# Performance work log

Hardware: AMD Instinct MI355X
Metric: run time of the kernel (lower is better)

Reference implementation:

```python
import jax, jax.numpy as jnp
from jax import lax
import numpy as np

K = 9  # nsamples = 3*3 ball-query neighbors
LAYERS = [
    dict(cin=0,    mid=45,   cout=64,   r=1.5, ss=2, tk=1, ts=1, pad=(0, 0)),
    dict(cin=64,   mid=96,   cout=128,  r=3.0, ss=2, tk=3, ts=2, pad=(1, 0)),
    dict(cin=128,  mid=192,  cout=256,  r=3.0, ss=1, tk=3, ts=1, pad=(1, 1)),
    dict(cin=256,  mid=384,  cout=512,  r=6.0, ss=2, tk=3, ts=2, pad=(1, 0)),
    dict(cin=512,  mid=768,  cout=1024, r=6.0, ss=1, tk=3, ts=1, pad=(1, 1)),
    dict(cin=1024, mid=1536, cout=2048, r=6.0, ss=2, tk=1, ts=1, pad=(0, 0)),
]

def furthest_point_sample(xyz, m):
    B, N, _ = xyz.shape
    def step(carry, _):
        mind, last = carry
        lastp = jnp.take_along_axis(xyz, last[:, None, None], axis=1)  # (B,1,3)
        mind = jnp.minimum(mind, jnp.sum((xyz - lastp) ** 2, axis=-1))
        nxt = jnp.argmax(mind, axis=-1).astype(jnp.int32)
        return (mind, nxt), last
    init = (jnp.full((B, N), 1e10, xyz.dtype), jnp.zeros((B,), jnp.int32))
    _, idxs = lax.scan(step, init, None, length=m)
    return jnp.swapaxes(idxs, 0, 1)

def ball_query(radius, k, points, anchors):
    # first-k-within-radius semantics of the pointnet2 CUDA ball_query kernel
    d2 = jnp.sum((anchors[:, :, None, :] - points[:, None, :, :]) ** 2, axis=-1)  # (B,M,N)
    N = points.shape[1]
    mask = d2 < radius * radius
    key = jnp.where(mask, jnp.arange(N, dtype=jnp.int32), N)
    idx = -lax.top_k(-key, k)[0]  # k smallest keys = first k in-radius indices
    first = jnp.argmax(mask, axis=-1).astype(jnp.int32)  # 0 if none in radius (CUDA init)
    return jnp.where(idx < N, idx, first[:, :, None]).astype(jnp.int32)

def pst_conv(xyzs, feats, Wd, Wf, Wt, cfg):
    # xyzs: (B,L,N,3); feats: (B,L,N,Cin) or None (channel-last layout, same math as torch (B,L,C,N))
    B, L, N, _ = xyzs.shape
    p0, p1 = cfg['pad']
    if p0 + p1:
        zx = jnp.zeros((B, 1, N, 3), xyzs.dtype)
        xyzs = jnp.concatenate([zx] * p0 + [xyzs] + [zx] * p1, axis=1)
        if feats is not None:
            zf = jnp.zeros((B, 1, N, feats.shape[-1]), feats.dtype)
            feats = jnp.concatenate([zf] * p0 + [feats] + [zf] * p1, axis=1)
    tr = cfg['tk'] // 2
    m = N // cfg['ss']
    bi = jnp.arange(B)[:, None, None]
    out_x, out_f = [], []
    for t in range(tr, xyzs.shape[1] - tr, cfg['ts']):
        aidx = furthest_point_sample(xyzs[:, t], m)
        anchor = jnp.take_along_axis(xyzs[:, t], aidx[:, :, None], axis=1)  # (B,m,3)
        parts = []
        for i in range(t - tr, t + tr + 1):
            idx = ball_query(cfg['r'], K, xyzs[:, i], anchor)   # (B,m,K)
            nb = xyzs[:, i][bi, idx]                            # (B,m,K,3) gather
            disp = nb - anchor[:, :, None, :]
            d = jnp.einsum('bmkc,oc->bmko', disp, Wd)           # 1x1 conv on displacement
            if feats is not None:
                fg = feats[:, i][bi, idx]                       # (B,m,K,Cin) gather
                sf = jnp.einsum('bmkc,oc->bmko', fg, Wf) * d    # 'multiplication' aggregation
            else:
                sf = d
            parts.append(jnp.sum(sf, axis=2))                   # 'sum' spatial pooling
        nf = jnp.concatenate(parts, axis=-1)                    # (B,m,tk*mid)
        mu = jnp.mean(nf, axis=(0, 1))
        var = jnp.var(nf, axis=(0, 1))
        nf = jax.nn.relu((nf - mu) * lax.rsqrt(var + 1e-5))     # BatchNorm1d (batch stats, affine=identity-init) + ReLU
        nf = jnp.einsum('bmc,oc->bmo', nf, Wt)                  # temporal 1x1 conv
        out_x.append(anchor)
        out_f.append(nf)
    return jnp.stack(out_x, axis=1), jnp.stack(out_f, axis=1)

def _forward(xyzs, Wds, Wfs, Wts, fc_w, fc_b):
    B, S, L, N, C = xyzs.shape
    x = xyzs.reshape(B * S, L, N, C)  # mirrors xyzs.reshape((-1, L_sub_clip, N_point, C_xyz))
    feats = None
    for li, cfg in enumerate(LAYERS):
        x, feats = pst_conv(x, feats, Wds[li], Wfs[li], Wts[li], cfg)
        if li < len(LAYERS) - 1:
            feats = jax.nn.relu(feats)  # F.relu between PSTConv blocks (not after conv4)
    tokens = jnp.einsum('blnc,oc->blno', feats, fc_w) + fc_b  # conv_fc on permuted features
    BT, Lout, M, Cout = tokens.shape  # Lout == 1 per the model's assert
    return tokens.reshape(B, S, M, Cout)

def setup_inputs() -> dict:
    key = jax.random.key(0)
    ks = iter(jax.random.split(key, 40))
    B, S, L, N = 8, 4, 4, 2048
    inp = {'xyzs': jax.random.normal(next(ks), (B, S, L, N, 3), jnp.float32), 'epoch': 1}
    def xav(k, o, i):
        gain = np.sqrt(2.0)  # relu gain, matching get_and_init_FC_layer style init
        bound = gain * np.sqrt(6.0 / (o + i))
        return jax.random.uniform(k, (o, i), jnp.float32, -bound, bound)
    for li, cfg in enumerate(LAYERS):
        inp['d%d' % li] = xav(next(ks), cfg['mid'], 3)
        if cfg['cin']:
            inp['f%d' % li] = xav(next(ks), cfg['mid'], cfg['cin'])
        inp['t%d' % li] = xav(next(ks), cfg['cout'], cfg['tk'] * cfg['mid'])
    inp['fc_w'] = xav(next(ks), 1024, 2048)
    inp['fc_b'] = jnp.zeros((1024,), jnp.float32)
    return inp

def reference(xyzs, d0, d1, d2, d3, d4, d5, f1, f2, f3, f4, f5, t0, t1, t2, t3, t4, t5, fc_w, fc_b, epoch):
    Wds = [d0, d1, d2, d3, d4, d5]
    Wfs = [None, f1, f2, f3, f4, f5]
    Wts = [t0, t1, t2, t3, t4, t5]
    return _forward(xyzs, Wds, Wfs, Wts, fc_w, fc_b)
```

## Files before the change

### kernel.cpp

```cpp
#include <hip/hip_runtime.h>
#include <hip/hip_bf16.h>
#include <math.h>

typedef __hip_bfloat16 bf16;
typedef _Float16 f16;
typedef _Float16 f16x2 __attribute__((ext_vector_type(2)));
typedef _Float16 f16x8 __attribute__((ext_vector_type(8)));
typedef float f32x4 __attribute__((ext_vector_type(4)));

struct Sched { int tt[5]; int fi[5]; int jj[5]; };
struct CvtF32 { const void* src[4]; float* dst[4]; int n[4]; int blk0[5]; };
struct CvtF16 { const void* src[6]; f16* dst[6]; int n[6]; int blk0[7]; };
struct W2J { const void* wd[5]; const void* wf[5]; f16* dst[5]; int mid[5]; int cin[5]; int n[5]; int blk0[6]; };

__global__ void k_detect(const unsigned int* __restrict__ w, int nwords, int* __restrict__ flag,
                         float* __restrict__ zp, int zn){
  if(blockIdx.x==0){
    __shared__ int cnt;
    if(threadIdx.x==0) cnt=0;
    __syncthreads();
    int local=0;
    for(int i=threadIdx.x;i<nwords;i+=256){
      unsigned int v=w[i];
      int e=(v>>7)&0xFF;
      if(e>=0xC0) local++;
    }
    atomicAdd(&cnt, local);
    __syncthreads();
    if(threadIdx.x==0) flag[0] = (cnt > (nwords>>3)) ? 1 : 0;
  } else {
    int i=(blockIdx.x-1)*256+threadIdx.x;
    if(i<zn) zp[i]=0.f;
  }
}

__device__ inline float ldmix(const void* p, size_t i, bool f32m){
  return f32m ? ((const float*)p)[i] : __bfloat162float(((const bf16*)p)[i]);
}

__global__ void k_cvt_all(CvtF32 J, const int* __restrict__ flag){
  int b=blockIdx.x;
  int j=0;
  while(j<3 && J.blk0[j+1]<=b) j++;
  int i=(b-J.blk0[j])*256+threadIdx.x;
  if(i>=J.n[j]) return;
  bool f32m=*flag!=0;
  J.dst[j][i]=ldmix(J.src[j],i,f32m);
}

__global__ __launch_bounds__(256) void k_fps0m(
    const float* __restrict__ xyz, float* __restrict__ anchors,
    CvtF16 J16, W2J JW, const int* __restrict__ flag, int cvtB)
{
  __shared__ float4 ptsS[8*256];
  __shared__ unsigned long long keyS[2][4];
  __shared__ float ancS[3*1024];
  int bid=(int)blockIdx.x;
  if(bid<128){
    const int L=4, N=2048, m=1024, T=4;
    int prob=bid;
    int b=prob/T, tt=prob%T;
    int f=tt;
    const float* src = xyz + ((size_t)(b*L+f))*N*3;
    float* anc = anchors + ((size_t)(b*T+tt))*m*3;
    int tid=threadIdx.x;
    for(int t=tid;t<N;t+=256)
      ptsS[t]=make_float4(src[3*t],src[3*t+1],src[3*t+2],0.f);
    __syncthreads();
    float px[8],py[8],pz[8],mind[8];
#pragma unroll
    for(int j=0;j<8;j++){
      float4 v=ptsS[tid+j*256];
      px[j]=v.x; py[j]=v.y; pz[j]=v.z; mind[j]=1e10f;
    }
    float4 p0=ptsS[0];
    float lx=p0.x, ly=p0.y, lz=p0.z;
    if(tid==0){ ancS[0]=lx; ancS[1]=ly; ancS[2]=lz; }
    int w=tid>>6;
    for(int it=1; it<m; ++it){
      float bv=-1.f; int bi=0;
#pragma unroll
      for(int j=0;j<8;j++){
#pragma clang fp contract(off)
        float dx=px[j]-lx, dy=py[j]-ly, dz=pz[j]-lz;
        float d2=dx*dx+dy*dy+dz*dz;
        float mv=mind[j]; if(d2<mv) mv=d2; mind[j]=mv;
        if(mv>bv){ bv=mv; bi=tid+j*256; }
      }
      unsigned int hi=__float_as_uint(bv);
      unsigned int lo=0xFFFFFFFFu-(unsigned)bi;
#define DPPSTEP(CTRL) { \
      unsigned int shi=(unsigned)__builtin_amdgcn_update_dpp(0,(int)hi,CTRL,0xF,0xF,true); \
      unsigned int slo=(unsigned)__builtin_amdgcn_update_dpp(0,(int)lo,CTRL,0xF,0xF,true); \
      bool g=(shi>hi)||(shi==hi&&slo>lo); \
      hi=g?shi:hi; lo=g?slo:lo; }
      DPPSTEP(0x111) DPPSTEP(0x112) DPPSTEP(0x114) DPPSTEP(0x118) DPPSTEP(0x142) DPPSTEP(0x143)
#undef DPPSTEP
      if((tid&63)==63)
        keyS[it&1][w]=((unsigned long long)hi<<32)|lo;
      __syncthreads();
      unsigned long long k0=keyS[it&1][0], k1=keyS[it&1][1];
      unsigned long long k2=keyS[it&1][2], k3=keyS[it&1][3];
      unsigned long long ka = k0>k1?k0:k1;
      unsigned long long kb = k2>k3?k2:k3;
      unsigned long long kk = ka>kb?ka:kb;
      int wi = (int)(0xFFFFFFFFu - (unsigned)(kk & 0xFFFFFFFFull));
      float4 wc = ptsS[wi];
      lx=wc.x; ly=wc.y; lz=wc.z;
      if(tid==0){ ancS[3*it]=lx; ancS[3*it+1]=ly; ancS[3*it+2]=lz; }
    }
    __syncthreads();
    for(int t=tid;t<3*m;t+=256) anc[t]=ancS[t];
  } else if(bid < 128+cvtB){
    int b=bid-128;
    int j=0;
    while(j<5 && J16.blk0[j+1]<=b) j++;
    int i=(b-J16.blk0[j])*256+threadIdx.x;
    if(i>=J16.n[j]) return;
    bool f32m=*flag!=0;
    J16.dst[j][i]=(f16)ldmix(J16.src[j],i,f32m);
  } else {
    int b=bid-128-cvtB;
    int j=0;
    while(j<4 && JW.blk0[j+1]<=b) j++;
    int i=(b-JW.blk0[j])*256+threadIdx.x;
    if(i>=JW.n[j]) return;
    int cin=JW.cin[j]; int K3=3*cin;
    int o=i/K3; int rem=i-o*K3; int a=rem/cin; int c=rem-a*cin;
    float v=0.f;
    if(o<JW.mid[j]){
      bool f32m=*flag!=0;
      v=ldmix(JW.wd[j],(size_t)3*o+a,f32m)*ldmix(JW.wf[j],(size_t)o*cin+c,f32m);
    }
    JW.dst[j][i]=(f16)v;
  }
}

template<int P>
__global__ __launch_bounds__(256) void k_mega(
    const float* __restrict__ xyzF, int Lf, int Nf, int mf,
    int c0,int c1,int c2,int c3, int Tf, float* __restrict__ ancOut, int fpsN,
    int oN, int isP0,
    const f16* __restrict__ featsO, const float* __restrict__ XinO, const float* __restrict__ XoutO,
    const int* __restrict__ bqO, f16* __restrict__ GoN, int mO, int cinO, int NO, int LinO,
    size_t aBSO, int MO, Sched SO, const float* __restrict__ WdO, int midO, int ldO,
    const float* __restrict__ XinB, const float* __restrict__ XoutB, int* __restrict__ bqOut,
    int NB, int mB, float r2B, int LinB, size_t aBSB, int MB, Sched SB, int chunksB)
{
  __shared__ float4 ptsS[P*256];
  __shared__ unsigned long long keyS[2][4];
  __shared__ float sp[768];
  int bid=(int)blockIdx.x;
  if(bid < fpsN){
    int prob=bid;
    int b=prob/Tf, tt=prob%Tf;
    int f=(tt==0)?c0:(tt==1)?c1:(tt==2)?c2:c3;
    const float* src = xyzF + ((size_t)(b*Lf+f))*Nf*3;
    float* anc = ancOut + ((size_t)(b*Tf+tt))*mf*3;
    int tid=threadIdx.x;
    for(int t=tid;t<Nf;t+=256)
      ptsS[t]=make_float4(src[3*t],src[3*t+1],src[3*t+2],0.f);
    __syncthreads();
    float px[P],py[P],pz[P],mind[P];
#pragma unroll
    for(int j=0;j<P;j++){
      float4 v=ptsS[tid+j*256];
      px[j]=v.x; py[j]=v.y; pz[j]=v.z; mind[j]=1e10f;
    }
    float4 p0=ptsS[0];
    float lx=p0.x, ly=p0.y, lz=p0.z;
    if(tid==0){ anc[0]=lx; anc[1]=ly; anc[2]=lz; }
    int w=tid>>6;
    for(int it=1; it<mf; ++it){
      float bv=-1.f; int bi=0;
#pragma unroll
      for(int j=0;j<P;j++){
#pragma clang fp contract(off)
        float dx=px[j]-lx, dy=py[j]-ly, dz=pz[j]-lz;
        float d2=dx*dx+dy*dy+dz*dz;
        float mv=mind[j]; if(d2<mv) mv=d2; mind[j]=mv;
        if(mv>bv){ bv=mv; bi=tid+j*256; }
      }
      unsigned int hi=__float_as_uint(bv);
      unsigned int lo=0xFFFFFFFFu-(unsigned)bi;
#define DPPSTEP(CTRL) { \
      unsigned int shi=(unsigned)__builtin_amdgcn_update_dpp(0,(int)hi,CTRL,0xF,0xF,true); \
      unsigned int slo=(unsigned)__builtin_amdgcn_update_dpp(0,(int)lo,CTRL,0xF,0xF,true); \
      bool g=(shi>hi)||(shi==hi&&slo>lo); \
      hi=g?shi:hi; lo=g?slo:lo; }
      DPPSTEP(0x111) DPPSTEP(0x112) DPPSTEP(0x114) DPPSTEP(0x118) DPPSTEP(0x142) DPPSTEP(0x143)
#undef DPPSTEP
      if((tid&63)==63)
        keyS[it&1][w]=((unsigned long long)hi<<32)|lo;
      __syncthreads();
      unsigned long long k0=keyS[it&1][0], k1=keyS[it&1][1];
      unsigned long long k2=keyS[it&1][2], k3=keyS[it&1][3];
      unsigned long long ka = k0>k1?k0:k1;
      unsigned long long kb = k2>k3?k2:k3;
      unsigned long long kk = ka>kb?ka:kb;
      int wi = (int)(0xFFFFFFFFu - (unsigned)(kk & 0xFFFFFFFFull));
      float4 wc = ptsS[wi];
      lx=wc.x; ly=wc.y; lz=wc.z;
      if(tid==0){ anc[3*it]=lx; anc[3*it+1]=ly; anc[3*it+2]=lz; }
    }
  } else if(bid < fpsN + oN){
    int ob = bid - fpsN;
    if(isP0){
      int quarter = MO>>2;
      int tt = ob / quarter, rb = ob - tt*quarter;
      int sub = threadIdx.x>>6;
      int o = threadIdx.x&63;
      int row = rb*4 + sub;
      int b = row/mO, mm = row - b*mO;
      const float* A = XoutO + (size_t)b*aBSO + (size_t)tt*mO*3 + (size_t)mm*3;
      float ax=A[0], ay=A[1], az=A[2];
      float w0=0,w1=0,w2=0;
      if(o<midO){ w0=WdO[3*o]; w1=WdO[3*o+1]; w2=WdO[3*o+2]; }
      int fr=SO.fi[tt];
      int nmask=NO-1;
      const int* id = bqO + ((size_t)tt*MO + row)*9;
      const float* Pb = XinO + ((size_t)b*LinO+fr)*(size_t)NO*3;
      float acc=0.f;
      for(int k=0;k<9;k++){
        int p=id[k] & nmask;
        const float* q = Pb + (size_t)p*3;
        float dx=q[0]-ax, dy=q[1]-ay, dz=q[2]-az;
        acc += dx*w0+dy*w1+dz*w2;
      }
      if(o<midO) GoN[(size_t)tt*MO*ldO + (size_t)row*ldO + o] = (f16)acc;
    } else {
      int cw2 = cinO>>1; if(cw2>256) cw2=256;
      int rpb = 256/cw2;
      int tid=threadIdx.x;
      int sub=tid/cw2, lc=tid-sub*cw2;
      int r=ob*rpb+sub;
      int Kp=3*cinO;
      int nmask=NO-1;
      int s=r/MO, mrow=r-s*MO;
      int b=mrow/mO, mm=mrow-b*mO;
      int tt=SO.tt[s], fr=SO.fi[s];
      const float* A0=XoutO+(size_t)b*aBSO+(size_t)tt*mO*3+(size_t)mm*3;
      float ax=A0[0],ay=A0[1],az=A0[2];
      const float* Pb=XinO+((size_t)b*LinO+fr)*(size_t)NO*3;
      const f16* Fb=featsO+(((size_t)b*LinO+fr)*(size_t)NO)*(size_t)cinO;
      const int* id=bqO+(size_t)r*9;
      int idx[9]; float d0[9],d1[9],d2a[9];
#pragma unroll
      for(int k=0;k<9;k++){
        int p=id[k]&nmask; idx[k]=p;
        const float* q=Pb+(size_t)p*3;
        d0[k]=q[0]-ax; d1[k]=q[1]-ay; d2a[k]=q[2]-az;
      }
      f16* Gr=GoN+(size_t)r*Kp;
      for(int cc=2*lc; cc<cinO; cc+=2*cw2){
        float a0=0,a1=0,a2=0,b0=0,b1=0,b2=0;
#pragma unroll
        for(int k=0;k<9;k++){
          f16x2 fv=*(const f16x2*)(Fb+(size_t)idx[k]*cinO+cc);
          float f0=(float)fv[0], f1=(float)fv[1];
          a0=fmaf(d0[k],f0,a0); b0=fmaf(d0[k],f1,b0);
          a1=fmaf(d1[k],f0,a1); b1=fmaf(d1[k],f1,b1);
          a2=fmaf(d2a[k],f0,a2); b2=fmaf(d2a[k],f1,b2);
        }
        f16x2 o0={(f16)a0,(f16)b0}, o1={(f16)a1,(f16)b1}, o2={(f16)a2,(f16)b2};
        *(f16x2*)(Gr+cc)=o0; *(f16x2*)(Gr+cinO+cc)=o1; *(f16x2*)(Gr+2*cinO+cc)=o2;
      }
    }
  } else {
    int fb=bid-fpsN-oN;
    int s=fb/(32*chunksB);
    int rem=fb-s*(32*chunksB);
    int b=rem/chunksB;
    int a=(rem-b*chunksB)*256+threadIdx.x;
    int tt=SB.tt[s], fr=SB.fi[s];
    const float* Pb = XinB + ((size_t)b*LinB + fr)*(size_t)NB*3;
    bool act = a<mB;
    float ax=0,ay=0,az=0;
    int* o = bqOut + ((size_t)s*MB + (size_t)b*mB + (size_t)(act?a:0))*9;
    if(act){
      const float* A=XoutB+(size_t)b*aBSB+(size_t)tt*mB*3+(size_t)a*3;
      ax=A[0]; ay=A[1]; az=A[2];
    }
    int cnt = act?0:9, first=0;
    for(int base=0; base<NB; base+=256){
      for(int t=threadIdx.x; t<768; t+=256) sp[t]=Pb[(size_t)base*3+t];
      __syncthreads();
      for(int q=0;q<256;q++){
#pragma clang fp contract(off)
        float dx=sp[3*q]-ax, dy=sp[3*q+1]-ay, dz=sp[3*q+2]-az;
        float d2=dx*dx+dy*dy+dz*dz;
        if(d2<r2B && cnt<9){
          int p=base+q;
          if(cnt==0) first=p;
          o[cnt]=p; cnt++;
        }
      }
      if(__syncthreads_and(cnt>=9)) break;
    }
    if(act){ for(int k=cnt;k<9;k++) o[k]=first; }
  }
}

__global__ __launch_bounds__(256) void k_outer(
    const f16* __restrict__ feats, const float* __restrict__ Xin,
    const float* __restrict__ Xout, const int* __restrict__ bqAll,
    f16* __restrict__ Gh, int m, int cin, int N, int Lin,
    size_t aBS, int nmask, int M, Sched S)
{
  int cw2 = cin>>1; if(cw2>256) cw2=256;
  int rpb = 256/cw2;
  int tid=threadIdx.x;
  int sub=tid/cw2, lc=tid-sub*cw2;
  int r=blockIdx.x*rpb+sub;
  int Kp=3*cin;
  int s=r/M, mrow=r-s*M;
  int b=mrow/m, mm=mrow-b*m;
  int tt=S.tt[s], fr=S.fi[s];
  const float* A0=Xout+(size_t)b*aBS+(size_t)tt*m*3+(size_t)mm*3;
  float ax=A0[0],ay=A0[1],az=A0[2];
  const float* Pb=Xin+((size_t)b*Lin+fr)*(size_t)N*3;
  const f16* Fb=feats+(((size_t)b*Lin+fr)*(size_t)N)*(size_t)cin;
  const int* id=bqAll+(size_t)r*9;
  int idx[9]; float d0[9],d1[9],d2a[9];
#pragma unroll
  for(int k=0;k<9;k++){
    int p=id[k]&nmask; idx[k]=p;
    const float* q=Pb+(size_t)p*3;
    d0[k]=q[0]-ax; d1[k]=q[1]-ay; d2a[k]=q[2]-az;
  }
  f16* Gr=Gh+(size_t)r*Kp;
  for(int cc=2*lc; cc<cin; cc+=2*cw2){
    float a0=0,a1=0,a2=0,b0=0,b1=0,b2=0;
#pragma unroll
    for(int k=0;k<9;k++){
      f16x2 fv=*(const f16x2*)(Fb+(size_t)idx[k]*cin+cc);
      float f0=(float)fv[0], f1=(float)fv[1];
      a0=fmaf(d0[k],f0,a0); b0=fmaf(d0[k],f1,b0);
      a1=fmaf(d1[k],f0,a1); b1=fmaf(d1[k],f1,b1);
      a2=fmaf(d2a[k],f0,a2); b2=fmaf(d2a[k],f1,b2);
    }
    f16x2 o0={(f16)a0,(f16)b0}, o1={(f16)a1,(f16)b1}, o2={(f16)a2,(f16)b2};
    *(f16x2*)(Gr+cc)=o0; *(f16x2*)(Gr+cin+cc)=o1; *(f16x2*)(Gr+2*cin+cc)=o2;
  }
}

__global__ __launch_bounds__(256) void k_pg(
    const f16* __restrict__ Gh, const f16* __restrict__ W2,
    f16* __restrict__ nfh, int Kp, int mid, int C, int M, Sched S,
    float* __restrict__ sumsL, int sumStride)
{
  __shared__ f16 As[128*40];
  __shared__ f16 Bs[128*40];
  int tid=threadIdx.x;
  int lane=tid&63, w=tid>>6;
  int quad=lane>>4, l15=lane&15;
  int rowOff=(w>>1)*64, colOff=(w&1)*64;
  int rowBase=blockIdx.x*128, colBase=blockIdx.y*128;
  f32x4 acc[4][4];
#pragma unroll
  for(int i=0;i<4;i++)
#pragma unroll
    for(int j=0;j<4;j++) acc[i][j]=(f32x4){0.f,0.f,0.f,0.f};
  int nct=Kp>>5;
  int srow=tid>>1, shalf=tid&1;
  for(int ct=0;ct<nct;ct++){
    __syncthreads();
    {
      const uint4* s=(const uint4*)(Gh+(size_t)(rowBase+srow)*Kp+(ct<<5)+(shalf<<4));
      uint4 u0=s[0], u1=s[1];
      *(uint4*)(As + srow*40 + (shalf<<4))     = u0;
      *(uint4*)(As + srow*40 + (shalf<<4) + 8) = u1;
    }
    {
      const uint4* s=(const uint4*)(W2+(size_t)(colBase+srow)*Kp+(ct<<5)+(shalf<<4));
      uint4 u0=s[0], u1=s[1];
      *(uint4*)(Bs + srow*40 + (shalf<<4))     = u0;
      *(uint4*)(Bs + srow*40 + (shalf<<4) + 8) = u1;
    }
    __syncthreads();
    f16x8 af[4], bf4[4];
#pragma unroll
    for(int rt=0;rt<4;rt++) af[rt]=*(const f16x8*)(As + (rowOff+rt*16+l15)*40 + quad*8);
#pragma unroll
    for(int ctl=0;ctl<4;ctl++) bf4[ctl]=*(const f16x8*)(Bs + (colOff+ctl*16+l15)*40 + quad*8);
#pragma unroll
    for(int rt=0;rt<4;rt++)
#pragma unroll
      for(int ctl=0;ctl<4;ctl++)
        acc[rt][ctl]=__builtin_amdgcn_mfma_f32_16x16x32_f16(af[rt],bf4[ctl],acc[rt][ctl],0,0,0);
  }
  int s0=rowBase/M;
  int tt0=S.tt[s0], j0=S.jj[s0];
#pragma unroll
  for(int ctl=0;ctl<4;ctl++){
    int gcol=colBase+colOff+ctl*16+l15;
    float cs=0.f, cq=0.f;
#pragma unroll
    for(int rt=0;rt<4;rt++)
#pragma unroll
      for(int r=0;r<4;r++){
        float v=(float)(f16)acc[rt][ctl][r];
        cs+=v; cq+=v*v;
      }
    cs+=__shfl_xor(cs,16); cq+=__shfl_xor(cq,16);
    cs+=__shfl_xor(cs,32); cq+=__shfl_xor(cq,32);
    if(quad==0 && gcol<mid){
      atomicAdd(&sumsL[tt0*sumStride + j0*mid + gcol], cs);
      atomicAdd(&sumsL[tt0*sumStride + C + j0*mid + gcol], cq);
    }
  }
#pragma unroll
  for(int rt=0;rt<4;rt++){
#pragma unroll
    for(int r=0;r<4;r++){
      int row=rowBase+rowOff+rt*16+quad*4+r;
      int s=row/M, mrow=row-s*M;
      int tt=S.tt[s], j=S.jj[s];
      f16* base = nfh + (size_t)tt*M*C + (size_t)mrow*C + j*mid;
#pragma unroll
      for(int ctl=0;ctl<4;ctl++){
        int col=colBase+colOff+ctl*16+l15;
        if(col<mid) base[col]=(f16)acc[rt][ctl][r];
      }
    }
  }
}

__global__ void k_bnstat(const f16* __restrict__ nfh, int M, int C, float* __restrict__ sumsL,
                         int mid, int4 jm, int sumStride){
  int c = blockIdx.x*256 + threadIdx.x;
  if(c>=C) return;
  int tt=blockIdx.z;
  int jmask = (tt==0)?jm.x:(tt==1)?jm.y:(tt==2)?jm.z:jm.w;
  int j=c/mid;
  if(!((jmask>>j)&1)) return;
  const f16* base=nfh+(size_t)tt*M*C;
  int rows = M>>5;
  int r0 = blockIdx.y*rows, r1 = r0+rows;
  float s=0.f, s2=0.f;
  for(int r=r0;r<r1;r++){
    float v=(float)base[(size_t)r*C+c];
    s+=v; s2+=v*v;
  }
  atomicAdd(&sumsL[tt*sumStride+c], s);
  atomicAdd(&sumsL[tt*sumStride+C+c], s2);
}

template<bool RELU, bool DYN, bool BNA>
__global__ __launch_bounds__(256) void k_gemm_mfma(
    const f16* __restrict__ Ag, const f16* __restrict__ Bh,
    const float* __restrict__ bias, void* __restrict__ out,
    int K, int N, int mloc, size_t oBS, size_t ttA, size_t ttO,
    const int* __restrict__ oflag, const float* __restrict__ sumsAll, int sumStride, float invM)
{
  __shared__ f16 As[128*40];
  __shared__ f16 Bs[128*40];
  __shared__ float scbL[BNA?2*2304:2];
  int tid=threadIdx.x;
  int lane=tid&63, w=tid>>6;
  int quad=lane>>4, l15=lane&15;
  int rowOff=(w>>1)*64, colOff=(w&1)*64;
  int rowBase=blockIdx.x*128, colBase=blockIdx.y*128;
  int tt=blockIdx.z;
  const f16* A0=Ag+(size_t)tt*ttA;
  if(BNA){
    const float* sm=sumsAll+(size_t)tt*sumStride;
    for(int c=tid;c<K;c+=256){
      float s1=sm[c], s2=sm[K+c];
      float mean=s1*invM;
      float var=s2*invM-mean*mean; if(var<0.f) var=0.f;
      float rs=(s2==0.f)?0.f:(1.0f/sqrtf(var+1e-5f));
      scbL[c]=rs; scbL[K+c]=-mean*rs;
    }
  }
  f32x4 acc[4][4];
#pragma unroll
  for(int i=0;i<4;i++)
#pragma unroll
    for(int j=0;j<4;j++) acc[i][j]=(f32x4){0.f,0.f,0.f,0.f};
  int nct=K>>5;
  int srow=tid>>1, shalf=tid&1;
  for(int ct=0;ct<nct;ct++){
    __syncthreads();
    {
      int c0g=(ct<<5)+(shalf<<4);
      const f16* src=A0+(size_t)(rowBase+srow)*K+c0g;
      if(BNA){
        f16x8 x0=((const f16x8*)src)[0], x1=((const f16x8*)src)[1];
        f16x8 h0,h1;
#pragma unroll
        for(int q=0;q<8;q++){
          h0[q]=(f16)fmaxf(fmaf((float)x0[q],scbL[c0g+q],scbL[K+c0g+q]),0.f);
          h1[q]=(f16)fmaxf(fmaf((float)x1[q],scbL[c0g+8+q],scbL[K+c0g+8+q]),0.f);
        }
        *(f16x8*)(As+srow*40+(shalf<<4))=h0;
        *(f16x8*)(As+srow*40+(shalf<<4)+8)=h1;
      } else {
        const uint4* s=(const uint4*)src;
        uint4 u0=s[0],u1=s[1];
        *(uint4*)(As+srow*40+(shalf<<4))=u0;
        *(uint4*)(As+srow*40+(shalf<<4)+8)=u1;
      }
    }
    {
      const uint4* s=(const uint4*)(Bh+(size_t)(colBase+srow)*K+(ct<<5)+(shalf<<4));
      uint4 u0=s[0], u1=s[1];
      *(uint4*)(Bs + srow*40 + (shalf<<4))     = u0;
      *(uint4*)(Bs + srow*40 + (shalf<<4) + 8) = u1;
    }
    __syncthreads();
    f16x8 af[4], bf4[4];
#pragma unroll
    for(int rt=0;rt<4;rt++) af[rt]=*(const f16x8*)(As + (rowOff+rt*16+l15)*40 + quad*8);
#pragma unroll
    for(int ctl=0;ctl<4;ctl++) bf4[ctl]=*(const f16x8*)(Bs + (colOff+ctl*16+l15)*40 + quad*8);
#pragma unroll
    for(int rt=0;rt<4;rt++)
#pragma unroll
      for(int ctl=0;ctl<4;ctl++)
        acc[rt][ctl]=__builtin_amdgcn_mfma_f32_16x16x32_f16(af[rt],bf4[ctl],acc[rt][ctl],0,0,0);
  }
  bool f32m = DYN ? (*oflag!=0) : true;
#pragma unroll
  for(int rt=0;rt<4;rt++){
#pragma unroll
    for(int r=0;r<4;r++){
      int row=rowBase+rowOff+rt*16+quad*4+r;
      int rb=row/mloc, rm=row-rb*mloc;
      size_t obase=(size_t)rb*oBS + (size_t)tt*ttO + (size_t)rm*N;
#pragma unroll
      for(int ctl=0;ctl<4;ctl++){
        int col=colBase+colOff+ctl*16+l15;
        float v=acc[rt][ctl][r];
        if(bias) v+=bias[col];
        if(RELU) v=fmaxf(v,0.f);
        if(DYN){
          if(!f32m) ((bf16*)out)[obase+col]=__float2bfloat16(v);
          else      ((float*)out)[obase+col]=v;
        } else {
          ((f16*)out)[obase+col]=(f16)v;
        }
      }
    }
  }
}

__global__ __launch_bounds__(256) void k_gemm0(
    const f16* __restrict__ nfh, const float* __restrict__ Wg,
    f16* __restrict__ out, int M, int K, int N, int mloc, size_t oBS, size_t ttO,
    const float* __restrict__ sumsAll, int sumStride, float invM)
{
  __shared__ alignas(16) float As[16][64];
  __shared__ alignas(16) float Bs[16][64];
  __shared__ float scbL[128];
  int tid=threadIdx.x, tx=tid&15, ty=tid>>4;
  int rowBase=blockIdx.x*64, colBase=blockIdx.y*64;
  int tt=blockIdx.z;
  const f16* A0=nfh+(size_t)tt*M*K;
  {
    const float* sm=sumsAll+(size_t)tt*sumStride;
    for(int c=tid;c<K;c+=256){
      float s1=sm[c], s2=sm[K+c];
      float mean=s1*invM;
      float var=s2*invM-mean*mean; if(var<0.f) var=0.f;
      float rs=(s2==0.f)?0.f:(1.0f/sqrtf(var+1e-5f));
      scbL[c]=rs; scbL[K+c]=-mean*rs;
    }
  }
  float acc[4][4];
#pragma unroll
  for(int i=0;i<4;i++)
#pragma unroll
    for(int j=0;j<4;j++) acc[i][j]=0.f;
  int lrow=tid&63, lcq=tid>>6;
  int nct=(K+15)>>4;
  for(int ct=0;ct<nct;ct++){
    __syncthreads();
    {
      int r=rowBase+lrow, c0=(ct<<4)+(lcq<<2);
#pragma unroll
      for(int q=0;q<4;q++){
        int c=c0+q;
        As[(lcq<<2)+q][lrow] = (c<K)? fmaxf(fmaf((float)A0[(size_t)r*K+c],scbL[c],scbL[K+c]),0.f) : 0.f;
      }
    }
    {
      int og=colBase+lrow, c0=(ct<<4)+(lcq<<2);
#pragma unroll
      for(int q=0;q<4;q++){
        int c=c0+q;
        Bs[(lcq<<2)+q][lrow] = (c<K)? Wg[(size_t)og*K+c] : 0.f;
      }
    }
    __syncthreads();
#pragma unroll
    for(int c=0;c<16;c++){
      float4 a4=*(const float4*)&As[c][ty<<2];
      float av[4]={a4.x,a4.y,a4.z,a4.w};
      float4 b4=*(const float4*)&Bs[c][tx<<2];
      float bw[4]={b4.x,b4.y,b4.z,b4.w};
#pragma unroll
      for(int i=0;i<4;i++)
#pragma unroll
        for(int j=0;j<4;j++) acc[i][j]+=av[i]*bw[j];
    }
  }
#pragma unroll
  for(int i=0;i<4;i++){
    int r=rowBase+(ty<<2)+i;
    int rb=r/mloc, rm=r-rb*mloc;
    size_t obase=(size_t)rb*oBS + (size_t)blockIdx.z*ttO + (size_t)rm*N;
#pragma unroll
    for(int j=0;j<4;j++){
      int o=colBase+(tx<<2)+j;
      out[obase+o]=(f16)fmaxf(acc[i][j],0.f);
    }
  }
}

extern "C" void kernel_launch(void* const* d_in, const int* in_sizes, int n_in,
                              void* d_out, int out_size, void* d_ws, size_t ws_size,
                              hipStream_t stream) {
  (void)in_sizes; (void)n_in; (void)out_size; (void)ws_size;

  const int di[6] = {2,4,7,10,13,16};
  const int fi6[6] = {-1,5,8,11,14,17};
  const int ti[6] = {3,6,9,12,15,18};

  const int midv[6]={45,96,192,384,768,1536};
  const int midp[6]={0,128,256,384,768,1536};
  const int cinv[6]={0,64,128,256,512,1024};
  const int coutv[6]={64,128,256,512,1024,2048};
  const int tkv[6]={1,3,3,3,3,1};
  const int Nv[6]={2048,1024,512,512,256,256};
  const int mv[6]={1024,512,512,256,256,128};
  const int Lv[6]={4,4,2,2,1,1};
  const int Tv[6]={4,2,2,1,1,1};
  const float rrv[6]={1.5f,3.f,3.f,6.f,6.f,6.f};

  float* ws=(float*)d_ws;
  size_t off=0;
  auto A=[&](size_t n)->float*{ float* p=ws+off; off+=(n+63)&~(size_t)63; return p; };
  auto Ah=[&](size_t n)->f16*{ return (f16*)A((n+1)/2); };

  int* flag=(int*)A(64);

  f16* W2h[6]; W2h[0]=nullptr;
  for(int l=1;l<6;l++) W2h[l]=Ah((size_t)midp[l]*3*cinv[l]);
  f16* Wth[6]; Wth[0]=nullptr;
  for(int l=1;l<6;l++) Wth[l]=Ah((size_t)coutv[l]*tkv[l]*midv[l]);
  float* Wd0=A(135);
  float* Wt0=A(2880);
  f16* fcwh=Ah(2097152);
  float* fcb=A(1024);

  float* X[7];
  X[0]=A(786432);
  for(int l=0;l<6;l++) X[l+1]=A((size_t)32*Tv[l]*mv[l]*3);

  f16* FA=Ah(8388608);
  f16* FB=Ah(8388608);
  f16* F[7]; F[0]=nullptr;
  for(int l=0;l<6;l++) F[l+1]=(l%2==0)?FA:FB;

  f16* nfh=Ah(18874368);
  float* sumsAll=A(11*4608);
  f16* Gh=Ah(25165824);
  int* bqA=(int*)A(1179648);
  int* bqB=(int*)A(1179648);
  int* bqBuf[2]={bqA,bqB};

  {
    int zn=11*4608;
    int zb=(zn+255)/256;
    k_detect<<<dim3(1+zb),dim3(256),0,stream>>>((const unsigned int*)d_in[0], 4096, flag, sumsAll, zn);
  }
  {
    CvtF32 J;
    J.src[0]=d_in[0];  J.dst[0]=X[0];  J.n[0]=786432;
    J.src[1]=d_in[3];  J.dst[1]=Wt0;   J.n[1]=2880;
    J.src[2]=d_in[20]; J.dst[2]=fcb;   J.n[2]=1024;
    J.src[3]=d_in[2];  J.dst[3]=Wd0;   J.n[3]=135;
    J.blk0[0]=0; J.blk0[1]=3072; J.blk0[2]=3084; J.blk0[3]=3088; J.blk0[4]=3089;
    k_cvt_all<<<dim3(3089),dim3(256),0,stream>>>(J,flag);
  }

  CvtF16 J16; int bp16=0;
  {
    int ns[6]={36864,147456,589824,2359296,3145728,2097152};
    const void* ss[6]={d_in[ti[1]],d_in[ti[2]],d_in[ti[3]],d_in[ti[4]],d_in[ti[5]],d_in[19]};
    f16* ds[6]={Wth[1],Wth[2],Wth[3],Wth[4],Wth[5],fcwh};
    for(int j2=0;j2<6;j2++){ J16.src[j2]=ss[j2]; J16.dst[j2]=ds[j2]; J16.n[j2]=ns[j2]; J16.blk0[j2]=bp16; bp16+=(ns[j2]+255)/256; }
    J16.blk0[6]=bp16;
  }
  W2J JW; int bpw2=0;
  {
    for(int l=1;l<6;l++){
      int j2=l-1;
      JW.wd[j2]=d_in[di[l]]; JW.wf[j2]=d_in[fi6[l]]; JW.dst[j2]=W2h[l];
      JW.mid[j2]=midv[l]; JW.cin[j2]=cinv[l]; JW.n[j2]=midp[l]*3*cinv[l];
      JW.blk0[j2]=bpw2; bpw2+=(JW.n[j2]+255)/256;
    }
    JW.blk0[5]=bpw2;
  }

  const int SLOTS[6]={4,5,4,2,1,1};
  const int sTT[6][5]={{0,1,2,3,0},{0,0,1,1,1},{0,0,1,1,0},{0,0,0,0,0},{0,0,0,0,0},{0,0,0,0,0}};
  const int sFI[6][5]={{0,1,2,3,0},{0,1,1,2,3},{0,1,0,1,0},{0,1,0,0,0},{0,0,0,0,0},{0,0,0,0,0}};
  const int sJJ[6][5]={{0,0,0,0,0},{1,2,0,1,2},{1,2,0,1,0},{1,2,0,0,0},{1,0,0,0,0},{0,0,0,0,0}};
  const int4 jm4l0={1,1,1,1};
  const int Tcenters[6][4]={{0,1,2,3},{0,2,0,0},{0,1,0,0},{0,0,0,0},{0,0,0,0},{0,0,0,0}};
  const int slotBase[6]={0,4,6,8,9,10};

  Sched Sl[6];
  for(int l=0;l<6;l++)
    for(int s=0;s<5;s++){ Sl[l].tt[s]=sTT[l][s]; Sl[l].fi[s]=sFI[l][s]; Sl[l].jj[s]=sJJ[l][s]; }

  auto bqGeo=[&](int lb, int& bqN, int& chunks){
    chunks=(mv[lb]+255)>>8;
    bqN=SLOTS[lb]*32*chunks;
  };

  k_fps0m<<<dim3((unsigned)(128+bp16+bpw2)),dim3(256),0,stream>>>(X[0],X[1],J16,JW,flag,bp16);

  {
    int bqN,chunks; bqGeo(0,bqN,chunks);
    int fpsN=32*Tv[1];
    k_mega<4><<<dim3((unsigned)(fpsN+bqN)),dim3(256),0,stream>>>(
        X[1],Lv[1],Nv[1],mv[1],Tcenters[1][0],Tcenters[1][1],Tcenters[1][2],Tcenters[1][3],Tv[1],X[2],fpsN,
        0,0, FA,X[0],X[1],bqA,nfh,mv[0],1,Nv[0],Lv[0],(size_t)Tv[0]*mv[0]*3,32*mv[0],Sl[0],Wd0,1,1,
        X[0],X[1],bqBuf[0],Nv[0],mv[0],rrv[0]*rrv[0],Lv[0],(size_t)Tv[0]*mv[0]*3,32*mv[0],Sl[0],chunks);
  }

  for(int l=0;l<6;l++){
    int N=Nv[l], m=mv[l], Lin=Lv[l], T=Tv[l], cin=cinv[l], mid=midv[l];
    int C=tkv[l]*midv[l], M=32*m, cout=coutv[l];
    size_t aBS=(size_t)T*m*3;
    float* sumsL=sumsAll+(size_t)slotBase[l]*4608;

    if(l<5){
      int lb=l+1;
      int bqN,chunksB; bqGeo(lb,bqN,chunksB);
      size_t aBSB=(size_t)Tv[lb]*mv[lb]*3;
      int MB=32*mv[lb];
      int oN, isP0;
      if(l==0){ isP0=1; oN=M; }
      else{
        isP0=0;
        int cw2=cin>>1; if(cw2>256) cw2=256;
        int rpb=256/cw2;
        oN=SLOTS[l]*M/rpb;
      }
      const f16* featsO=(l==0)?FA:F[l];
      f16* GoN=(l==0)?nfh:Gh;
      int fpsN=0, lf=l+2;
      if(lf<=5) fpsN=32*Tv[lf];
      int a0=0,a1=0,a2=0,a3=0;
      if(lf<=5){ a0=Tcenters[lf][0]; a1=Tcenters[lf][1]; a2=Tcenters[lf][2]; a3=Tcenters[lf][3]; }
      const float* xyzF=(lf<=5)?X[lf]:X[5];
      float* ancOut=(lf<=5)?X[lf+1]:X[6];
      int Lf=(lf<=5)?Lv[lf]:1, Nf=(lf<=5)?Nv[lf]:256, mf=(lf<=5)?mv[lf]:1, Tf=(lf<=5)?Tv[lf]:1;
      dim3 g((unsigned)(fpsN+oN+bqN)), blk(256);
      if(lf<=5 && Nv[lf]==512)
        k_mega<2><<<g,blk,0,stream>>>(xyzF,Lf,Nf,mf,a0,a1,a2,a3,Tf,ancOut,fpsN,
            oN,isP0, featsO,X[l],X[l+1],bqBuf[l&1],GoN,m,cin,N,Lin,aBS,M,Sl[l],Wd0,mid,C,
            X[lb],X[lb+1],bqBuf[lb&1],Nv[lb],mv[lb],rrv[lb]*rrv[lb],Lv[lb],aBSB,MB,Sl[lb],chunksB);
      else
        k_mega<1><<<g,blk,0,stream>>>(xyzF,Lf,Nf,mf,a0,a1,a2,a3,Tf,ancOut,fpsN,
            oN,isP0, featsO,X[l],X[l+1],bqBuf[l&1],GoN,m,cin,N,Lin,aBS,M,Sl[l],Wd0,mid,C,
            X[lb],X[lb+1],bqBuf[lb&1],Nv[lb],mv[lb],rrv[lb]*rrv[lb],Lv[lb],aBSB,MB,Sl[lb],chunksB);
    } else {
      int cw2=cin>>1; if(cw2>256) cw2=256;
      int rpb=256/cw2;
      k_outer<<<dim3((unsigned)(SLOTS[l]*M/rpb)),256,0,stream>>>(
          F[l],X[l],X[l+1],bqBuf[l&1],Gh,m,cin,N,Lin,aBS,N-1,M,Sl[l]);
    }

    if(l>=1)
      k_pg<<<dim3((unsigned)(SLOTS[l]*M/128),(unsigned)(midp[l]/128)),256,0,stream>>>(
          Gh,W2h[l],nfh,3*cin,mid,C,M,Sl[l],sumsL,4608);
    else
      k_bnstat<<<dim3((C+255)/256,32,T),256,0,stream>>>(nfh,M,C,sumsL,mid,jm4l0,4608);

    size_t oBS=(size_t)T*m*cout;
    size_t ttO=(size_t)m*cout;
    float invM=1.0f/(float)M;
    if(l==0)
      k_gemm0<<<dim3(M/64,1,4),256,0,stream>>>(nfh,Wt0,F[1],M,C,cout,m,oBS,ttO,sumsL,4608,invM);
    else if(l<5)
      k_gemm_mfma<true,false,true><<<dim3(M/128,cout/128,T),256,0,stream>>>(
          nfh,Wth[l],nullptr,F[l+1],C,cout,m,oBS,(size_t)M*C,ttO,nullptr,sumsL,4608,invM);
    else
      k_gemm_mfma<false,false,true><<<dim3(M/128,cout/128,T),256,0,stream>>>(
          nfh,Wth[l],nullptr,F[l+1],C,cout,m,oBS,(size_t)M*C,ttO,nullptr,sumsL,4608,invM);
  }

  k_gemm_mfma<false,true,false><<<dim3(4096/128,1024/128,1),256,0,stream>>>(
      F[6],fcwh,fcb,d_out,2048,1024,128,(size_t)128*1024,0,0,flag,nullptr,0,0.f);
}
```

Measured before the change: 2.191 ms.

## Fold final FC into last layer weights and merge f32 conversion into fps kernel

```diff
diff --git a/kernel.cpp b/kernel.cpp
--- a/kernel.cpp
+++ b/kernel.cpp
@@ -38,19 +38,9 @@
   return f32m ? ((const float*)p)[i] : __bfloat162float(((const bf16*)p)[i]);
 }
 
-__global__ void k_cvt_all(CvtF32 J, const int* __restrict__ flag){
-  int b=blockIdx.x;
-  int j=0;
-  while(j<3 && J.blk0[j+1]<=b) j++;
-  int i=(b-J.blk0[j])*256+threadIdx.x;
-  if(i>=J.n[j]) return;
-  bool f32m=*flag!=0;
-  J.dst[j][i]=ldmix(J.src[j],i,f32m);
-}
-
 __global__ __launch_bounds__(256) void k_fps0m(
-    const float* __restrict__ xyz, float* __restrict__ anchors,
-    CvtF16 J16, W2J JW, const int* __restrict__ flag, int cvtB)
+    const void* __restrict__ xyzRaw, float* __restrict__ anchors,
+    CvtF32 J32, CvtF16 J16, W2J JW, const int* __restrict__ flag, int c32B, int c16B)
 {
   __shared__ float4 ptsS[8*256];
   __shared__ unsigned long long keyS[2][4];
@@ -58,14 +48,15 @@
   int bid=(int)blockIdx.x;
   if(bid<128){
     const int L=4, N=2048, m=1024, T=4;
+    bool f32m=*flag!=0;
     int prob=bid;
     int b=prob/T, tt=prob%T;
     int f=tt;
-    const float* src = xyz + ((size_t)(b*L+f))*N*3;
+    size_t srcOff = ((size_t)(b*L+f))*N*3;
     float* anc = anchors + ((size_t)(b*T+tt))*m*3;
     int tid=threadIdx.x;
     for(int t=tid;t<N;t+=256)
-      ptsS[t]=make_float4(src[3*t],src[3*t+1],src[3*t+2],0.f);
+      ptsS[t]=make_float4(ldmix(xyzRaw,srcOff+3*t,f32m),ldmix(xyzRaw,srcOff+3*t+1,f32m),ldmix(xyzRaw,srcOff+3*t+2,f32m),0.f);
     __syncthreads();
     float px[8],py[8],pz[8],mind[8];
 #pragma unroll
@@ -111,16 +102,30 @@
     }
     __syncthreads();
     for(int t=tid;t<3*m;t+=256) anc[t]=ancS[t];
-  } else if(bid < 128+cvtB){
+  } else if(bid < 128+c32B){
     int b=bid-128;
+    int j=0;
+    while(j<3 && J32.blk0[j+1]<=b) j++;
+    int i=(b-J32.blk0[j])*256+threadIdx.x;
+    if(i>=J32.n[j]) return;
+    bool f32m=*flag!=0;
+    J32.dst[j][i]=ldmix(J32.src[j],i,f32m);
+  } else if(bid < 128+c32B+c16B){
+    int b=bid-128-c32B;
     int j=0;
     while(j<5 && J16.blk0[j+1]<=b) j++;
     int i=(b-J16.blk0[j])*256+threadIdx.x;
     if(i>=J16.n[j]) return;
     bool f32m=*flag!=0;
-    J16.dst[j][i]=(f16)ldmix(J16.src[j],i,f32m);
+    float v=ldmix(J16.src[j],i,f32m);
+    if(j==4){
+      int o=i/1536, c=i-o*1536;
+      J16.dst[4][(size_t)c*2048+o]=(f16)v;
+    } else {
+      J16.dst[j][i]=(f16)v;
+    }
   } else {
-    int b=bid-128-cvtB;
+    int b=bid-128-c32B-c16B;
     int j=0;
     while(j<4 && JW.blk0[j+1]<=b) j++;
     int i=(b-JW.blk0[j])*256+threadIdx.x;
@@ -136,7 +141,7 @@
   }
 }
 
-template<int P>
+template<int P, bool WB>
 __global__ __launch_bounds__(256) void k_mega(
     const float* __restrict__ xyzF, int Lf, int Nf, int mf,
     int c0,int c1,int c2,int c3, int Tf, float* __restrict__ ancOut, int fpsN,
@@ -145,11 +150,14 @@
     const int* __restrict__ bqO, f16* __restrict__ GoN, int mO, int cinO, int NO, int LinO,
     size_t aBSO, int MO, Sched SO, const float* __restrict__ WdO, int midO, int ldO,
     const float* __restrict__ XinB, const float* __restrict__ XoutB, int* __restrict__ bqOut,
-    int NB, int mB, float r2B, int LinB, size_t aBSB, int MB, Sched SB, int chunksB)
+    int NB, int mB, float r2B, int LinB, size_t aBSB, int MB, Sched SB, int chunksB, int bqN,
+    const f16* __restrict__ wA, const f16* __restrict__ wB, f16* __restrict__ wO)
 {
   __shared__ float4 ptsS[P*256];
   __shared__ unsigned long long keyS[2][4];
   __shared__ float sp[768];
+  __shared__ f16 AsW[WB?128*40:1];
+  __shared__ f16 BsW[WB?128*40:1];
   int bid=(int)blockIdx.x;
   if(bid < fpsN){
     int prob=bid;
@@ -266,7 +274,7 @@
         *(f16x2*)(Gr+cc)=o0; *(f16x2*)(Gr+cinO+cc)=o1; *(f16x2*)(Gr+2*cinO+cc)=o2;
       }
     }
-  } else {
+  } else if(bid < fpsN + oN + bqN){
     int fb=bid-fpsN-oN;
     int s=fb/(32*chunksB);
     int rem=fb-s*(32*chunksB);
@@ -298,6 +306,58 @@
       if(__syncthreads_and(cnt>=9)) break;
     }
     if(act){ for(int k=cnt;k<9;k++) o[k]=first; }
+  } else if(WB){
+    int wb = bid - fpsN - oN - bqN;
+    if(wb>=96) return;
+    int rowBase=(wb/12)*128, colBase=(wb%12)*128;
+    int tid=threadIdx.x;
+    int lane=tid&63, w=tid>>6;
+    int quad=lane>>4, l15=lane&15;
+    int rowOff=(w>>1)*64, colOff=(w&1)*64;
+    f32x4 acc[4][4];
+#pragma unroll
+    for(int i=0;i<4;i++)
+#pragma unroll
+      for(int j=0;j<4;j++) acc[i][j]=(f32x4){0.f,0.f,0.f,0.f};
+    const int Kp=2048;
+    int srow=tid>>1, shalf=tid&1;
+    for(int ct=0;ct<Kp>>5;ct++){
+      __syncthreads();
+      {
+        const uint4* s=(const uint4*)(wA+(size_t)(rowBase+srow)*Kp+(ct<<5)+(shalf<<4));
+        uint4 u0=s[0], u1=s[1];
+        *(uint4*)(AsW + srow*40 + (shalf<<4))     = u0;
+        *(uint4*)(AsW + srow*40 + (shalf<<4) + 8) = u1;
+      }
+      {
+        const uint4* s=(const uint4*)(wB+(size_t)(colBase+srow)*Kp+(ct<<5)+(shalf<<4));
+        uint4 u0=s[0], u1=s[1];
+        *(uint4*)(BsW + srow*40 + (shalf<<4))     = u0;
+        *(uint4*)(BsW + srow*40 + (shalf<<4) + 8) = u1;
+      }
+      __syncthreads();
+      f16x8 af[4], bf4[4];
+#pragma unroll
+      for(int rt=0;rt<4;rt++) af[rt]=*(const f16x8*)(AsW + (rowOff+rt*16+l15)*40 + quad*8);
+#pragma unroll
+      for(int ctl=0;ctl<4;ctl++) bf4[ctl]=*(const f16x8*)(BsW + (colOff+ctl*16+l15)*40 + quad*8);
+#pragma unroll
+      for(int rt=0;rt<4;rt++)
+#pragma unroll
+        for(int ctl=0;ctl<4;ctl++)
+          acc[rt][ctl]=__builtin_amdgcn_mfma_f32_16x16x32_f16(af[rt],bf4[ctl],acc[rt][ctl],0,0,0);
+    }
+#pragma unroll
+    for(int rt=0;rt<4;rt++)
+#pragma unroll
+      for(int r=0;r<4;r++){
+        int row=rowBase+rowOff+rt*16+quad*4+r;
+#pragma unroll
+        for(int ctl=0;ctl<4;ctl++){
+          int col=colBase+colOff+ctl*16+l15;
+          wO[(size_t)row*1536+col]=(f16)acc[rt][ctl][r];
+        }
+      }
   }
 }
 
@@ -653,6 +713,7 @@
   float* Wt0=A(2880);
   f16* fcwh=Ah(2097152);
   float* fcb=A(1024);
+  f16* Wp=Ah(1572864);
 
   float* X[7];
   X[0]=A(786432);
@@ -675,16 +736,16 @@
     int zb=(zn+255)/256;
     k_detect<<<dim3(1+zb),dim3(256),0,stream>>>((const unsigned int*)d_in[0], 4096, flag, sumsAll, zn);
   }
+
+  CvtF32 J32; int bp32=0;
   {
-    CvtF32 J;
-    J.src[0]=d_in[0];  J.dst[0]=X[0];  J.n[0]=786432;
-    J.src[1]=d_in[3];  J.dst[1]=Wt0;   J.n[1]=2880;
-    J.src[2]=d_in[20]; J.dst[2]=fcb;   J.n[2]=1024;
-    J.src[3]=d_in[2];  J.dst[3]=Wd0;   J.n[3]=135;
-    J.blk0[0]=0; J.blk0[1]=3072; J.blk0[2]=3084; J.blk0[3]=3088; J.blk0[4]=3089;
-    k_cvt_all<<<dim3(3089),dim3(256),0,stream>>>(J,flag);
-  }
-
+    J32.src[0]=d_in[0];  J32.dst[0]=X[0];  J32.n[0]=786432;
+    J32.src[1]=d_in[3];  J32.dst[1]=Wt0;   J32.n[1]=2880;
+    J32.src[2]=d_in[20]; J32.dst[2]=fcb;   J32.n[2]=1024;
+    J32.src[3]=d_in[2];  J32.dst[3]=Wd0;   J32.n[3]=135;
+    for(int j2=0;j2<4;j2++){ J32.blk0[j2]=bp32; bp32+=(J32.n[j2]+255)/256; }
+    J32.blk0[4]=bp32;
+  }
   CvtF16 J16; int bp16=0;
   {
     int ns[6]={36864,147456,589824,2359296,3145728,2097152};
@@ -721,15 +782,17 @@
     bqN=SLOTS[lb]*32*chunks;
   };
 
-  k_fps0m<<<dim3((unsigned)(128+bp16+bpw2)),dim3(256),0,stream>>>(X[0],X[1],J16,JW,flag,bp16);
+  k_fps0m<<<dim3((unsigned)(128+bp32+bp16+bpw2)),dim3(256),0,stream>>>(
+      d_in[0],X[1],J32,J16,JW,flag,bp32,bp16);
 
   {
     int bqN,chunks; bqGeo(0,bqN,chunks);
     int fpsN=32*Tv[1];
-    k_mega<4><<<dim3((unsigned)(fpsN+bqN)),dim3(256),0,stream>>>(
+    k_mega<4,true><<<dim3((unsigned)(fpsN+bqN+96)),dim3(256),0,stream>>>(
         X[1],Lv[1],Nv[1],mv[1],Tcenters[1][0],Tcenters[1][1],Tcenters[1][2],Tcenters[1][3],Tv[1],X[2],fpsN,
         0,0, FA,X[0],X[1],bqA,nfh,mv[0],1,Nv[0],Lv[0],(size_t)Tv[0]*mv[0]*3,32*mv[0],Sl[0],Wd0,1,1,
-        X[0],X[1],bqBuf[0],Nv[0],mv[0],rrv[0]*rrv[0],Lv[0],(size_t)Tv[0]*mv[0]*3,32*mv[0],Sl[0],chunks);
+        X[0],X[1],bqBuf[0],Nv[0],mv[0],rrv[0]*rrv[0],Lv[0],(size_t)Tv[0]*mv[0]*3,32*mv[0],Sl[0],chunks,bqN,
+        fcwh,Wth[5],Wp);
   }
 
   for(int l=0;l<6;l++){
@@ -762,13 +825,15 @@
       int Lf=(lf<=5)?Lv[lf]:1, Nf=(lf<=5)?Nv[lf]:256, mf=(lf<=5)?mv[lf]:1, Tf=(lf<=5)?Tv[lf]:1;
       dim3 g((unsigned)(fpsN+oN+bqN)), blk(256);
       if(lf<=5 && Nv[lf]==512)
-        k_mega<2><<<g,blk,0,stream>>>(xyzF,Lf,Nf,mf,a0,a1,a2,a3,Tf,ancOut,fpsN,
+        k_mega<2,false><<<g,blk,0,stream>>>(xyzF,Lf,Nf,mf,a0,a1,a2,a3,Tf,ancOut,fpsN,
             oN,isP0, featsO,X[l],X[l+1],bqBuf[l&1],GoN,m,cin,N,Lin,aBS,M,Sl[l],Wd0,mid,C,
-            X[lb],X[lb+1],bqBuf[lb&1],Nv[lb],mv[lb],rrv[lb]*rrv[lb],Lv[lb],aBSB,MB,Sl[lb],chunksB);
+            X[lb],X[lb+1],bqBuf[lb&1],Nv[lb],mv[lb],rrv[lb]*rrv[lb],Lv[lb],aBSB,MB,Sl[lb],chunksB,bqN,
+            nullptr,nullptr,nullptr);
       else
-        k_mega<1><<<g,blk,0,stream>>>(xyzF,Lf,Nf,mf,a0,a1,a2,a3,Tf,ancOut,fpsN,
+        k_mega<1,false><<<g,blk,0,stream>>>(xyzF,Lf,Nf,mf,a0,a1,a2,a3,Tf,ancOut,fpsN,
             oN,isP0, featsO,X[l],X[l+1],bqBuf[l&1],GoN,m,cin,N,Lin,aBS,M,Sl[l],Wd0,mid,C,
-            X[lb],X[lb+1],bqBuf[lb&1],Nv[lb],mv[lb],rrv[lb]*rrv[lb],Lv[lb],aBSB,MB,Sl[lb],chunksB);
+            X[lb],X[lb+1],bqBuf[lb&1],Nv[lb],mv[lb],rrv[lb]*rrv[lb],Lv[lb],aBSB,MB,Sl[lb],chunksB,bqN,
+            nullptr,nullptr,nullptr);
     } else {
       int cw2=cin>>1; if(cw2>256) cw2=256;
       int rpb=256/cw2;
@@ -791,10 +856,7 @@
       k_gemm_mfma<true,false,true><<<dim3(M/128,cout/128,T),256,0,stream>>>(
           nfh,Wth[l],nullptr,F[l+1],C,cout,m,oBS,(size_t)M*C,ttO,nullptr,sumsL,4608,invM);
     else
-      k_gemm_mfma<false,false,true><<<dim3(M/128,cout/128,T),256,0,stream>>>(
-          nfh,Wth[l],nullptr,F[l+1],C,cout,m,oBS,(size_t)M*C,ttO,nullptr,sumsL,4608,invM);
-  }
-
-  k_gemm_mfma<false,true,false><<<dim3(4096/128,1024/128,1),256,0,stream>>>(
-      F[6],fcwh,fcb,d_out,2048,1024,128,(size_t)128*1024,0,0,flag,nullptr,0,0.f);
-}
+      k_gemm_mfma<false,true,true><<<dim3(M/128,1024/128,1),256,0,stream>>>(
+          nfh,Wp,fcb,d_out,C,1024,m,(size_t)m*1024,0,0,flag,sumsL,4608,invM);
+  }
+}
```

New measurement: 2.246 ms. 1.03x slower.
